# Kernel optimization log

Hardware: AMD Instinct MI355X
Metric: run time of the kernel (lower is better)

The kernel has to match this reference:

```python
import jax, jax.numpy as jnp
import numpy as np

N, F, H = 4096, 512, 64
TEMP = 1.0
EPS = 1e-6


def _lin_init(k, fi, fo):
    s = 1.0 / np.sqrt(fi)
    return jax.random.uniform(k, (fi, fo), jnp.float32, -s, s)


def setup_inputs() -> dict:
    key = jax.random.key(0)
    ks = jax.random.split(key, 8)
    adj = jax.random.uniform(ks[0], (N, N), jnp.float32)
    adj = 0.5 * (adj + adj.T)  # symmetric dense adjacency
    x = jax.random.normal(ks[1], (N, F), jnp.float32)
    return {
        'adj': adj,
        'x': x,
        'Wg': _lin_init(ks[2], F, H), 'bg': jnp.zeros((H,), jnp.float32),
        'Wa1': _lin_init(ks[3], H, H), 'ba1': jnp.zeros((H,), jnp.float32),
        'Wa2': _lin_init(ks[4], H, F), 'ba2': jnp.zeros((F,), jnp.float32),
        'Wx1': _lin_init(ks[5], H, H), 'bx1': jnp.zeros((H,), jnp.float32),
        'Wx2': _lin_init(ks[6], H, F), 'bx2': jnp.zeros((F,), jnp.float32),
    }


def _relaxed_bernoulli_st(probs, noise_logistic, temp):
    # pyro RelaxedBernoulliStraightThrough.rsample(): gumbel-sigmoid + hard round w/ ST grad
    p = jnp.clip(probs, EPS, 1.0 - EPS)
    logits = jnp.log(p) - jnp.log1p(-p)
    soft = jax.nn.sigmoid((logits + noise_logistic) / temp)
    hard = jnp.round(soft)
    return soft + jax.lax.stop_gradient(hard - soft)


def _logistic_noise(k, shape):
    u = jax.random.uniform(k, shape, jnp.float32, EPS, 1.0 - EPS)
    return jnp.log(u) - jnp.log1p(-u)


def reference(adj, x, Wg, bg, Wa1, ba1, Wa2, ba2, Wx1, bx1, Wx2, bx2):
    nkey = jax.random.key(42)
    k1, k2 = jax.random.split(nkey)
    # GCN_Body, 1 layer (dropout is eval no-op): h = relu(A @ (X W) + b)
    h = jax.nn.relu(adj @ (x @ Wg) + bg)            # [N, H]
    # MLPA: Z = Linear(ReLU(Linear(h)))
    Z = jax.nn.relu(h @ Wa1 + ba1) @ Wa2 + ba2      # [N, F]
    adj_logits = Z @ Z.T                            # [N, N]
    edge_probs = jax.nn.sigmoid(adj_logits)
    a = _relaxed_bernoulli_st(edge_probs, _logistic_noise(k1, (N, N)), TEMP)
    a = jnp.triu(a, 1)
    a = a + a.T
    # normalize_adj: fill_diagonal_(1); D^{-1/2} A D^{-1/2} (diag matmuls == row/col scaling)
    i = jnp.arange(N)
    a = a.at[i, i].set(1.0)
    d = a.sum(1) ** -0.5                            # [N]
    adj_norm = d[:, None] * a * d[None, :]
    # MLPX feature mask
    mask_logits = jax.nn.relu(h @ Wx1 + bx1) @ Wx2 + bx2  # [N, F]
    mask_probs = jax.nn.sigmoid(mask_logits)
    mask = _relaxed_bernoulli_st(mask_probs, _logistic_noise(k2, (N, F)), TEMP)
    x_new = x * mask
    return (adj_norm, x_new, adj_logits)
```

## Files before the change

### kernel.cpp

```cpp
#include <hip/hip_runtime.h>
#include <cstdint>
#include <cmath>

#define NN 4096
#define FF 512
#define HH 64
#define KSPLIT 8

typedef unsigned short ushort_t;
typedef short bf16x8 __attribute__((ext_vector_type(8)));
typedef float f32x4 __attribute__((ext_vector_type(4)));

__host__ __device__ __forceinline__ uint32_t rotl32(uint32_t x, int r) {
    return (x << r) | (x >> (32 - r));
}

__host__ __device__ __forceinline__ void threefry2x32(uint32_t ks0, uint32_t ks1,
                                                      uint32_t x0, uint32_t x1,
                                                      uint32_t& o0, uint32_t& o1) {
    uint32_t ks2 = ks0 ^ ks1 ^ 0x1BD11BDAu;
    x0 += ks0; x1 += ks1;
    x0 += x1; x1 = rotl32(x1, 13); x1 ^= x0;
    x0 += x1; x1 = rotl32(x1, 15); x1 ^= x0;
    x0 += x1; x1 = rotl32(x1, 26); x1 ^= x0;
    x0 += x1; x1 = rotl32(x1,  6); x1 ^= x0;
    x0 += ks1; x1 += ks2 + 1u;
    x0 += x1; x1 = rotl32(x1, 17); x1 ^= x0;
    x0 += x1; x1 = rotl32(x1, 29); x1 ^= x0;
    x0 += x1; x1 = rotl32(x1, 16); x1 ^= x0;
    x0 += x1; x1 = rotl32(x1, 24); x1 ^= x0;
    x0 += ks2; x1 += ks0 + 2u;
    x0 += x1; x1 = rotl32(x1, 13); x1 ^= x0;
    x0 += x1; x1 = rotl32(x1, 15); x1 ^= x0;
    x0 += x1; x1 = rotl32(x1, 26); x1 ^= x0;
    x0 += x1; x1 = rotl32(x1,  6); x1 ^= x0;
    x0 += ks0; x1 += ks1 + 3u;
    x0 += x1; x1 = rotl32(x1, 17); x1 ^= x0;
    x0 += x1; x1 = rotl32(x1, 29); x1 ^= x0;
    x0 += x1; x1 = rotl32(x1, 16); x1 ^= x0;
    x0 += x1; x1 = rotl32(x1, 24); x1 ^= x0;
    x0 += ks1; x1 += ks2 + 4u;
    x0 += x1; x1 = rotl32(x1, 13); x1 ^= x0;
    x0 += x1; x1 = rotl32(x1, 15); x1 ^= x0;
    x0 += x1; x1 = rotl32(x1, 26); x1 ^= x0;
    x0 += x1; x1 = rotl32(x1,  6); x1 ^= x0;
    x0 += ks2; x1 += ks0 + 5u;
    o0 = x0; o1 = x1;
}

__device__ __forceinline__ uint32_t jax_bits32(uint32_t k0, uint32_t k1, uint32_t j) {
    uint32_t b0, b1;
    threefry2x32(k0, k1, 0u, j, b0, b1);
    return b0 ^ b1;
}

__device__ __forceinline__ float jax_uniform(uint32_t bits) {
    const float minv = 1e-6f;
    const float maxv = (float)(1.0 - 1e-6);
    const float span = maxv - minv;
    float f = __uint_as_float((bits >> 9) | 0x3f800000u) - 1.0f;
    float u = __fadd_rn(__fmul_rn(f, span), minv);
    return fmaxf(minv, u);
}

__device__ __forceinline__ float hard_sample_f(float l, float u) {
    float thr = 1.0f / (1.0f + expf(l));
    return (u > thr) ? 1.0f : 0.0f;
}

__device__ __forceinline__ ushort_t f32_to_bf16_rne(float f) {
    uint32_t x = __float_as_uint(f);
    uint32_t r = (x + 0x7fffu + ((x >> 16) & 1u)) >> 16;
    return (ushort_t)r;
}


__global__ void k_xw(const float* __restrict__ x, const float* __restrict__ Wg,
                     ushort_t* __restrict__ Tt) {
    __shared__ ushort_t Tls[4][64];
    int col = threadIdx.x, ty = threadIdx.y;
    int row = blockIdx.x * 4 + ty;
    const float* xr = x + row * FF;
    float acc = 0.0f;
    #pragma unroll 4
    for (int k = 0; k < FF; ++k)
        acc += xr[k] * Wg[k * HH + col];
    Tls[ty][col] = f32_to_bf16_rne(acc);
    __syncthreads();
    int t = ty * 64 + col;
    if (t < 64) {
        uint2 v;
        ushort_t* p = (ushort_t*)&v;
        p[0] = Tls[0][t]; p[1] = Tls[1][t]; p[2] = Tls[2][t]; p[3] = Tls[3][t];
        *(uint2*)&Tt[(size_t)t * NN + blockIdx.x * 4] = v;
    }
}

__global__ void __launch_bounds__(256)
k_adjT_mfma(const float* __restrict__ adj, const ushort_t* __restrict__ Tt,
            float* __restrict__ partial) {
    __shared__ __align__(16) ushort_t As[64][72];
    __shared__ __align__(16) ushort_t Tl[64][72];
    int t = threadIdx.x;
    int lane = t & 63, w = t >> 6;
    int lr = lane & 15, lk = lane >> 4;
    int r0 = blockIdx.x * 64;
    int kb = blockIdx.y * (NN / KSPLIT);
    f32x4 acc[4] = {};
    for (int k0 = 0; k0 < NN / KSPLIT; k0 += 64) {
        __syncthreads();
        #pragma unroll
        for (int i = 0; i < 4; ++i) {
            int idx = t + i * 256;
            int rr = idx >> 4;
            int kq = (idx & 15) * 4;
            float4 v = *(const float4*)&adj[(size_t)(r0 + rr) * NN + kb + k0 + kq];
            uint32_t lo = (uint32_t)f32_to_bf16_rne(v.x) | ((uint32_t)f32_to_bf16_rne(v.y) << 16);
            uint32_t hi = (uint32_t)f32_to_bf16_rne(v.z) | ((uint32_t)f32_to_bf16_rne(v.w) << 16);
            uint2 pk = {lo, hi};
            *(uint2*)&As[rr][kq] = pk;
        }
        #pragma unroll
        for (int i = 0; i < 2; ++i) {
            int idx = t + i * 256;
            int cc = idx >> 3;
            int kq = (idx & 7) * 8;
            *(uint4*)&Tl[cc][kq] = *(const uint4*)&Tt[(size_t)cc * NN + kb + k0 + kq];
        }
        __syncthreads();
        #pragma unroll
        for (int ks = 0; ks < 2; ++ks) {
            bf16x8 a = *(const bf16x8*)&As[w * 16 + lr][ks * 32 + lk * 8];
            #pragma unroll
            for (int c = 0; c < 4; ++c) {
                bf16x8 bb = *(const bf16x8*)&Tl[c * 16 + lr][ks * 32 + lk * 8];
                acc[c] = __builtin_amdgcn_mfma_f32_16x16x32_bf16(a, bb, acc[c], 0, 0, 0);
            }
        }
    }
    float* P = partial + (size_t)blockIdx.y * NN * HH;
    #pragma unroll
    for (int c = 0; c < 4; ++c)
        #pragma unroll
        for (int reg = 0; reg < 4; ++reg)
            P[(size_t)(r0 + w * 16 + lk * 4 + reg) * HH + c * 16 + lr] = acc[c][reg];
}

__global__ void k_hred(const float* __restrict__ partial, const float* __restrict__ bg,
                       float* __restrict__ h) {
    int idx = blockIdx.x * 256 + threadIdx.x;
    float s = 0.0f;
    #pragma unroll
    for (int p = 0; p < KSPLIT; ++p) s += partial[(size_t)p * NN * HH + idx];
    float v = s + bg[idx & (HH - 1)];
    h[idx] = v > 0.0f ? v : 0.0f;
}

__global__ void __launch_bounds__(256)
k_mlpZ(const float* __restrict__ h, const float* __restrict__ W1,
       const float* __restrict__ b1, const float* __restrict__ W2,
       const float* __restrict__ b2, ushort_t* __restrict__ Zb) {
    __shared__ float W1l[HH][HH];
    __shared__ float A1l[8][HH];
    __shared__ float hl[8][HH];
    int t = threadIdx.x;
    int r0 = blockIdx.x * 8;
    for (int n = t; n < HH * HH; n += 256) ((float*)W1l)[n] = W1[n];
    for (int n = t; n < 8 * HH; n += 256) ((float*)hl)[n] = h[r0 * HH + n];
    __syncthreads();
    {
        int col = t & 63;
        int rb = t >> 6;
        #pragma unroll
        for (int rr = 0; rr < 2; ++rr) {
            int row = rb * 2 + rr;
            float acc = b1[col];
            #pragma unroll
            for (int k = 0; k < HH; ++k) acc += hl[row][k] * W1l[k][col];
            A1l[row][col] = acc > 0.0f ? acc : 0.0f;
        }
    }
    __syncthreads();
    #pragma unroll
    for (int p = 0; p < 2; ++p) {
        int col = p * 256 + t;
        float wc[HH];
        #pragma unroll
        for (int k = 0; k < HH; ++k) wc[k] = W2[k * FF + col];
        float bb = b2[col];
        #pragma unroll
        for (int row = 0; row < 8; ++row) {
            float acc = bb;
            #pragma unroll
            for (int k = 0; k < HH; ++k) acc += A1l[row][k] * wc[k];
            Zb[(size_t)(r0 + row) * FF + col] = f32_to_bf16_rne(acc);
        }
    }
}

__global__ void __launch_bounds__(256)
k_mlpM(const float* __restrict__ h, const float* __restrict__ W1,
       const float* __restrict__ b1, const float* __restrict__ W2,
       const float* __restrict__ b2, const float* __restrict__ x,
       float* __restrict__ xnew, uint32_t k20, uint32_t k21,
       float Lmin, float Lmax) {
    __shared__ float W1l[HH][HH];
    __shared__ float A1l[8][HH];
    __shared__ float hl[8][HH];
    int t = threadIdx.x;
    int r0 = blockIdx.x * 8;
    for (int n = t; n < HH * HH; n += 256) ((float*)W1l)[n] = W1[n];
    for (int n = t; n < 8 * HH; n += 256) ((float*)hl)[n] = h[r0 * HH + n];
    __syncthreads();
    {
        int col = t & 63;
        int rb = t >> 6;
        #pragma unroll
        for (int rr = 0; rr < 2; ++rr) {
            int row = rb * 2 + rr;
            float acc = b1[col];
            #pragma unroll
            for (int k = 0; k < HH; ++k) acc += hl[row][k] * W1l[k][col];
            A1l[row][col] = acc > 0.0f ? acc : 0.0f;
        }
    }
    __syncthreads();
    #pragma unroll
    for (int p = 0; p < 2; ++p) {
        int col = p * 256 + t;
        float wc[HH];
        #pragma unroll
        for (int k = 0; k < HH; ++k) wc[k] = W2[k * FF + col];
        float bb = b2[col];
        #pragma unroll
        for (int row = 0; row < 8; ++row) {
            float acc = bb;
            #pragma unroll
            for (int k = 0; k < HH; ++k) acc += A1l[row][k] * wc[k];
            float ml = acc;
            float l = ml < Lmin ? Lmin : (ml > Lmax ? Lmax : ml);
            uint32_t idx = (uint32_t)(r0 + row) * FF + (uint32_t)col;
            float u = jax_uniform(jax_bits32(k20, k21, idx));
            float m = hard_sample_f(l, u);
            size_t gi = (size_t)(r0 + row) * FF + col;
            xnew[gi] = (m != 0.0f) ? x[gi] : 0.0f;
        }
    }
}

__global__ void __launch_bounds__(256)
k_zzt_gemm_tri(const ushort_t* __restrict__ Zb, float* __restrict__ out2) {
    __shared__ __align__(16) union {
        struct { ushort_t At[128][72]; ushort_t Bt[128][72]; } s;
        float Tls[32][132];
    } sm;
    int t = threadIdx.x;
    int lane = t & 63, w = t >> 6;
    int lr = lane & 15, lk = lane >> 4;
    int b = blockIdx.x, bi = 0;
    while (b >= 32 - bi) { b -= 32 - bi; ++bi; }
    int bj = bi + b;
    int rbase = bi * 128, cbase = bj * 128;
    f32x4 acc[2][8] = {};
    for (int k0 = 0; k0 < FF; k0 += 64) {
        __syncthreads();
        for (int n = t; n < 1024; n += 256) {
            int rr = n >> 3, ck = n & 7;
            *(uint4*)&sm.s.At[rr][ck * 8] = *(const uint4*)&Zb[(size_t)(rbase + rr) * FF + k0 + ck * 8];
            *(uint4*)&sm.s.Bt[rr][ck * 8] = *(const uint4*)&Zb[(size_t)(cbase + rr) * FF + k0 + ck * 8];
        }
        __syncthreads();
        #pragma unroll
        for (int ks = 0; ks < 2; ++ks) {
            bf16x8 a0 = *(const bf16x8*)&sm.s.At[w * 32 + lr][ks * 32 + lk * 8];
            bf16x8 a1 = *(const bf16x8*)&sm.s.At[w * 32 + 16 + lr][ks * 32 + lk * 8];
            #pragma unroll
            for (int j = 0; j < 8; ++j) {
                bf16x8 bb = *(const bf16x8*)&sm.s.Bt[j * 16 + lr][ks * 32 + lk * 8];
                acc[0][j] = __builtin_amdgcn_mfma_f32_16x16x32_bf16(a0, bb, acc[0][j], 0, 0, 0);
                acc[1][j] = __builtin_amdgcn_mfma_f32_16x16x32_bf16(a1, bb, acc[1][j], 0, 0, 0);
            }
        }
    }
    #pragma unroll
    for (int it = 0; it < 2; ++it) {
        int rg = rbase + w * 32 + it * 16 + lk * 4;
        #pragma unroll
        for (int reg = 0; reg < 4; ++reg)
            #pragma unroll
            for (int j = 0; j < 8; ++j)
                out2[(size_t)(rg + reg) * NN + cbase + j * 16 + lr] = acc[it][j][reg];
    }
    if (bi != bj) {
        #pragma unroll
        for (int g = 0; g < 4; ++g) {
            __syncthreads();
            #pragma unroll
            for (int it = 0; it < 2; ++it)
                #pragma unroll
                for (int jp = 0; jp < 2; ++jp)
                    #pragma unroll
                    for (int reg = 0; reg < 4; ++reg)
                        sm.Tls[jp * 16 + lr][w * 32 + it * 16 + lk * 4 + reg] =
                            acc[it][g * 2 + jp][reg];
            __syncthreads();
            #pragma unroll
            for (int r4 = 0; r4 < 4; ++r4) {
                int tr = r4 * 8 + (t >> 5);
                int tc = (t & 31) * 4;
                float4 v = *(const float4*)&sm.Tls[tr][tc];
                *(float4*)&out2[(size_t)(cbase + g * 32 + tr) * NN + rbase + tc] = v;
            }
        }
    }
}

__global__ void __launch_bounds__(512)
k_sample_tri(const float* __restrict__ out2, uint32_t* __restrict__ mask,
             float* __restrict__ rowsum, uint32_t k10, uint32_t k11,
             float Lmin, float Lmax) {
    __shared__ uint32_t Wl[128][5];
    __shared__ int rs[128], cs[128];
    int t = threadIdx.x;
    int b = blockIdx.x, bi = 0;
    while (b >= 32 - bi) { b -= 32 - bi; ++bi; }
    int bj = bi + b;
    int rbase = bi * 128, cbase = bj * 128;
    if (t < 128) { rs[t] = 0; cs[t] = 0; }
    __syncthreads();
    int rr = t >> 2, wc = t & 3;
    int r = rbase + rr;
    const float* zr = out2 + (size_t)r * NN + cbase + wc * 32;
    uint32_t word = 0;
    #pragma unroll
    for (int q = 0; q < 8; ++q) {
        float4 zv = *(const float4*)&zr[q * 4];
        float za[4] = {zv.x, zv.y, zv.z, zv.w};
        #pragma unroll
        for (int e4 = 0; e4 < 4; ++e4) {
            int e = q * 4 + e4;
            int c = cbase + wc * 32 + e;
            float z = za[e4];
            float l = z < Lmin ? Lmin : (z > Lmax ? Lmax : z);
            int lo = r < c ? r : c;
            int hi = r < c ? c : r;
            uint32_t idx = (uint32_t)lo * NN + (uint32_t)hi;
            float u = jax_uniform(jax_bits32(k10, k11, idx));
            float thr = 1.0f / (1.0f + expf(l));
            uint32_t bit = (r == c) ? 1u : (u > thr ? 1u : 0u);
            word |= bit << e;
        }
    }
    Wl[rr][wc] = word;
    mask[(size_t)r * (NN / 32) + ((cbase >> 5) + wc)] = word;
    atomicAdd(&rs[rr], (int)__popc(word));
    __syncthreads();
    if (bi != bj) {
        int cc = t >> 2, wr = t & 3;
        uint32_t tw = 0;
        #pragma unroll
        for (int bb = 0; bb < 32; ++bb)
            tw |= ((Wl[wr * 32 + bb][cc >> 5] >> (cc & 31)) & 1u) << bb;
        mask[(size_t)(cbase + cc) * (NN / 32) + ((rbase >> 5) + wr)] = tw;
        atomicAdd(&cs[cc], (int)__popc(tw));
    }
    __syncthreads();
    if (t < 128) {
        atomicAdd(&rowsum[rbase + t], (float)rs[t]);
        if (bi != bj) atomicAdd(&rowsum[cbase + t], (float)cs[t]);
    }
}

__global__ void k_scale3(const uint32_t* __restrict__ mask,
                         const float* __restrict__ rowsum, float* __restrict__ out0) {
    size_t idx = ((size_t)blockIdx.x * 256 + threadIdx.x) * 4;
    int r = (int)(idx >> 12);
    int c = (int)(idx & 4095);
    uint32_t wv = mask[idx >> 5];
    int sh = (int)(idx & 31);
    float dr = 1.0f / sqrtf(rowsum[r]);
    float4 rc = *(const float4*)&rowsum[c];
    float4 o;
    o.x = ((wv >> (sh + 0)) & 1u) ? dr * (1.0f / sqrtf(rc.x)) : 0.0f;
    o.y = ((wv >> (sh + 1)) & 1u) ? dr * (1.0f / sqrtf(rc.y)) : 0.0f;
    o.z = ((wv >> (sh + 2)) & 1u) ? dr * (1.0f / sqrtf(rc.z)) : 0.0f;
    o.w = ((wv >> (sh + 3)) & 1u) ? dr * (1.0f / sqrtf(rc.w)) : 0.0f;
    *(float4*)&out0[idx] = o;
}

extern "C" void kernel_launch(void* const* d_in, const int* in_sizes, int n_in,
                              void* d_out, int out_size, void* d_ws, size_t ws_size,
                              hipStream_t stream) {
    const float* adj = (const float*)d_in[0];
    const float* x   = (const float*)d_in[1];
    const float* Wg  = (const float*)d_in[2];
    const float* bg  = (const float*)d_in[3];
    const float* Wa1 = (const float*)d_in[4];
    const float* ba1 = (const float*)d_in[5];
    const float* Wa2 = (const float*)d_in[6];
    const float* ba2 = (const float*)d_in[7];
    const float* Wx1 = (const float*)d_in[8];
    const float* bx1 = (const float*)d_in[9];
    const float* Wx2 = (const float*)d_in[10];
    const float* bx2 = (const float*)d_in[11];

    float* out0 = (float*)d_out;
    float* out1 = out0 + (size_t)NN * NN;
    float* out2 = out1 + (size_t)NN * FF;

    ushort_t* Tt   = (ushort_t*)d_ws;
    float* h       = (float*)((char*)d_ws + (1 << 20));
    ushort_t* Zb   = (ushort_t*)(h + NN * HH);
    float* partial = (float*)((char*)Zb + (size_t)NN * FF * 2);
    float* rowsum  = partial + (size_t)KSPLIT * NN * HH;
    uint32_t* mask = (uint32_t*)partial;

    uint32_t k1a, k1b, k2a, k2b;
    threefry2x32(0u, 42u, 0u, 0u, k1a, k1b);
    threefry2x32(0u, 42u, 0u, 1u, k2a, k2b);

    const float Lmax = (float)(std::log(1.0 - 1e-6) - std::log1p(-(1.0 - 1e-6)));
    const float Lmin = (float)(std::log(1e-6) - std::log1p(-1e-6));

    k_xw<<<NN / 4, dim3(64, 4), 0, stream>>>(x, Wg, Tt);
    k_adjT_mfma<<<dim3(64, KSPLIT), 256, 0, stream>>>(adj, Tt, partial);
    k_hred<<<NN * HH / 256, 256, 0, stream>>>(partial, bg, h);
    k_mlpZ<<<NN / 8, 256, 0, stream>>>(h, Wa1, ba1, Wa2, ba2, Zb);

    k_zzt_gemm_tri<<<528, 256, 0, stream>>>(Zb, out2);

    hipMemsetAsync(rowsum, 0, NN * sizeof(float), stream);
    k_sample_tri<<<528, 512, 0, stream>>>(out2, mask, rowsum, k1a, k1b, Lmin, Lmax);
    k_scale3<<<NN * NN / 4 / 256, 256, 0, stream>>>(mask, rowsum, out0);

    k_mlpM<<<NN / 8, 256, 0, stream>>>(h, Wx1, bx1, Wx2, bx2, x, out1,
                                       k2a, k2b, Lmin, Lmax);
}
```

Baseline: 393.9 us.

## Fuse Bernoulli edge sampling into the triangular ZZ^T GEMM epilogue

```diff
diff --git a/kernel.cpp b/kernel.cpp
--- a/kernel.cpp
+++ b/kernel.cpp
@@ -249,14 +249,19 @@
 }
 
 __global__ void __launch_bounds__(256)
-k_zzt_gemm_tri(const ushort_t* __restrict__ Zb, float* __restrict__ out2) {
+k_zzt_fused(const ushort_t* __restrict__ Zb, float* __restrict__ out2,
+            uint32_t* __restrict__ mask, float* __restrict__ rowsum,
+            uint32_t k10, uint32_t k11, float Lmin, float Lmax) {
     __shared__ __align__(16) union {
         struct { ushort_t At[128][72]; ushort_t Bt[128][72]; } s;
         float Tls[32][132];
     } sm;
+    __shared__ uint32_t Wl[128][5];
+    __shared__ int rs_i[128], cs_i[128];
     int t = threadIdx.x;
     int lane = t & 63, w = t >> 6;
     int lr = lane & 15, lk = lane >> 4;
+    if (t < 128) { rs_i[t] = 0; cs_i[t] = 0; }
     int b = blockIdx.x, bi = 0;
     while (b >= 32 - bi) { b -= 32 - bi; ++bi; }
     int bj = bi + b;
@@ -291,19 +296,19 @@
             for (int j = 0; j < 8; ++j)
                 out2[(size_t)(rg + reg) * NN + cbase + j * 16 + lr] = acc[it][j][reg];
     }
-    if (bi != bj) {
-        #pragma unroll
-        for (int g = 0; g < 4; ++g) {
-            __syncthreads();
-            #pragma unroll
-            for (int it = 0; it < 2; ++it)
+    #pragma unroll 1
+    for (int g = 0; g < 4; ++g) {
+        __syncthreads();
+        #pragma unroll
+        for (int it = 0; it < 2; ++it)
+            #pragma unroll
+            for (int jp = 0; jp < 2; ++jp)
                 #pragma unroll
-                for (int jp = 0; jp < 2; ++jp)
-                    #pragma unroll
-                    for (int reg = 0; reg < 4; ++reg)
-                        sm.Tls[jp * 16 + lr][w * 32 + it * 16 + lk * 4 + reg] =
-                            acc[it][g * 2 + jp][reg];
-            __syncthreads();
+                for (int reg = 0; reg < 4; ++reg)
+                    sm.Tls[jp * 16 + lr][w * 32 + it * 16 + lk * 4 + reg] =
+                        acc[it][g * 2 + jp][reg];
+        __syncthreads();
+        if (bi != bj) {
             #pragma unroll
             for (int r4 = 0; r4 < 4; ++r4) {
                 int tr = r4 * 8 + (t >> 5);
@@ -312,62 +317,51 @@
                 *(float4*)&out2[(size_t)(cbase + g * 32 + tr) * NN + rbase + tc] = v;
             }
         }
-    }
-}
-
-__global__ void __launch_bounds__(512)
-k_sample_tri(const float* __restrict__ out2, uint32_t* __restrict__ mask,
-             float* __restrict__ rowsum, uint32_t k10, uint32_t k11,
-             float Lmin, float Lmax) {
-    __shared__ uint32_t Wl[128][5];
-    __shared__ int rs[128], cs[128];
-    int t = threadIdx.x;
-    int b = blockIdx.x, bi = 0;
-    while (b >= 32 - bi) { b -= 32 - bi; ++bi; }
-    int bj = bi + b;
-    int rbase = bi * 128, cbase = bj * 128;
-    if (t < 128) { rs[t] = 0; cs[t] = 0; }
-    __syncthreads();
-    int rr = t >> 2, wc = t & 3;
-    int r = rbase + rr;
-    const float* zr = out2 + (size_t)r * NN + cbase + wc * 32;
-    uint32_t word = 0;
-    #pragma unroll
-    for (int q = 0; q < 8; ++q) {
-        float4 zv = *(const float4*)&zr[q * 4];
-        float za[4] = {zv.x, zv.y, zv.z, zv.w};
-        #pragma unroll
-        for (int e4 = 0; e4 < 4; ++e4) {
-            int e = q * 4 + e4;
-            int c = cbase + wc * 32 + e;
-            float z = za[e4];
-            float l = z < Lmin ? Lmin : (z > Lmax ? Lmax : z);
-            int lo = r < c ? r : c;
-            int hi = r < c ? c : r;
-            uint32_t idx = (uint32_t)lo * NN + (uint32_t)hi;
-            float u = jax_uniform(jax_bits32(k10, k11, idx));
-            float thr = 1.0f / (1.0f + expf(l));
-            uint32_t bit = (r == c) ? 1u : (u > thr ? 1u : 0u);
-            word |= bit << e;
-        }
-    }
-    Wl[rr][wc] = word;
-    mask[(size_t)r * (NN / 32) + ((cbase >> 5) + wc)] = word;
-    atomicAdd(&rs[rr], (int)__popc(word));
+        {
+            int rr = t >> 1, half = t & 1;
+            int r = rbase + rr;
+            uint32_t hw = 0;
+            #pragma unroll
+            for (int e = 0; e < 16; ++e) {
+                int cl = half * 16 + e;
+                float z = sm.Tls[cl][rr];
+                int c = cbase + g * 32 + cl;
+                float l = z < Lmin ? Lmin : (z > Lmax ? Lmax : z);
+                int lo = r < c ? r : c;
+                int hi = r < c ? c : r;
+                uint32_t idx = (uint32_t)lo * NN + (uint32_t)hi;
+                float u = jax_uniform(jax_bits32(k10, k11, idx));
+                float thr = 1.0f / (1.0f + expf(l));
+                uint32_t bit = (r == c) ? 1u : (u > thr ? 1u : 0u);
+                hw |= bit << e;
+            }
+            uint32_t p = (uint32_t)__shfl_xor((int)hw, 1);
+            if (half == 0) {
+                uint32_t word = hw | (p << 16);
+                Wl[rr][g] = word;
+                mask[(size_t)r * (NN / 32) + (cbase >> 5) + g] = word;
+                atomicAdd(&rs_i[rr], (int)__popc(word));
+            }
+        }
+    }
     __syncthreads();
     if (bi != bj) {
-        int cc = t >> 2, wr = t & 3;
-        uint32_t tw = 0;
-        #pragma unroll
-        for (int bb = 0; bb < 32; ++bb)
-            tw |= ((Wl[wr * 32 + bb][cc >> 5] >> (cc & 31)) & 1u) << bb;
-        mask[(size_t)(cbase + cc) * (NN / 32) + ((rbase >> 5) + wr)] = tw;
-        atomicAdd(&cs[cc], (int)__popc(tw));
+        int cc = t >> 1;
+        #pragma unroll
+        for (int wi = 0; wi < 2; ++wi) {
+            int wr = (t & 1) * 2 + wi;
+            uint32_t tw = 0;
+            #pragma unroll
+            for (int bb = 0; bb < 32; ++bb)
+                tw |= ((Wl[wr * 32 + bb][cc >> 5] >> (cc & 31)) & 1u) << bb;
+            mask[(size_t)(cbase + cc) * (NN / 32) + (rbase >> 5) + wr] = tw;
+            atomicAdd(&cs_i[cc], (int)__popc(tw));
+        }
     }
     __syncthreads();
     if (t < 128) {
-        atomicAdd(&rowsum[rbase + t], (float)rs[t]);
-        if (bi != bj) atomicAdd(&rowsum[cbase + t], (float)cs[t]);
+        atomicAdd(&rowsum[rbase + t], (float)rs_i[t]);
+        if (bi != bj) atomicAdd(&rowsum[cbase + t], (float)cs_i[t]);
     }
 }
 
@@ -427,10 +421,9 @@
     k_hred<<<NN * HH / 256, 256, 0, stream>>>(partial, bg, h);
     k_mlpZ<<<NN / 8, 256, 0, stream>>>(h, Wa1, ba1, Wa2, ba2, Zb);
 
-    k_zzt_gemm_tri<<<528, 256, 0, stream>>>(Zb, out2);
-
     hipMemsetAsync(rowsum, 0, NN * sizeof(float), stream);
-    k_sample_tri<<<528, 512, 0, stream>>>(out2, mask, rowsum, k1a, k1b, Lmin, Lmax);
+    k_zzt_fused<<<528, 256, 0, stream>>>(Zb, out2, mask, rowsum,
+                                         k1a, k1b, Lmin, Lmax);
     k_scale3<<<NN * NN / 4 / 256, 256, 0, stream>>>(mask, rowsum, out0);
 
     k_mlpM<<<NN / 8, 256, 0, stream>>>(h, Wx1, bx1, Wx2, bx2, x, out1,
```

After: 471.4 us. 1.2x slower.
